# Optimization experiments

Hardware: AMD Instinct MI355X
Metric: run time of the kernel (lower is better)

The kernel has to match this reference:

```python
import jax, jax.numpy as jnp
import numpy as np

CONV_LAYERS = 1
BI_GRU_LAYERS = 2
BN_EPS = 1e-3


def _bn(x, gamma, beta, mean, var):
    return gamma * (x - mean) * jax.lax.rsqrt(var + BN_EPS) + beta


def _gru_pass(x, Wx, Wh, b_in, b_rec, reverse=False):
    # Keras GRU: reset_after=True, recurrent_activation=sigmoid, activation=relu,
    # gate order [z, r, h]. x: [B,T,D] -> [B,T,U]
    B, T, _ = x.shape
    U = Wh.shape[0]
    if reverse:
        x = x[:, ::-1]
    xg = jnp.einsum('btd,dg->btg', x, Wx) + b_in  # [B,T,3U] input-side gates, precomputed
    xg = jnp.swapaxes(xg, 0, 1)                    # time-major [T,B,3U]

    def step(h, g):
        rg = h @ Wh + b_rec                        # recurrent-side gates [B,3U]
        xz, xr, xh = jnp.split(g, 3, axis=-1)
        rz, rr, rh = jnp.split(rg, 3, axis=-1)
        z = jax.nn.sigmoid(xz + rz)
        r = jax.nn.sigmoid(xr + rr)
        hh = jax.nn.relu(xh + r * rh)              # reset_after: r gates the recurrent term
        h = z * h + (1.0 - z) * hh
        return h, h

    h0 = jnp.zeros((B, U), x.dtype)
    _, hs = jax.lax.scan(step, h0, xg)             # [T,B,U]
    hs = jnp.swapaxes(hs, 0, 1)
    if reverse:
        hs = hs[:, ::-1]
    return hs


def setup_inputs() -> dict:
    key = jax.random.key(0)
    ks = jax.random.split(key, 16)
    B, T, F = 32, 1024, 80
    C, U, V, K = 512, 512, 1024, 11
    s = 0.02
    inp = {
        'x': jax.random.normal(ks[0], (B, T, F), jnp.float32),
        'conv_w': jax.random.normal(ks[1], (K, F, C), jnp.float32) * s,
        'conv_b': jnp.zeros((C,), jnp.float32),
        'gru_fwd_wx': jax.random.normal(ks[2], (C, 3 * U), jnp.float32) * s,
        'gru_fwd_wh': jax.random.normal(ks[3], (U, 3 * U), jnp.float32) * s,
        'gru_fwd_bi': jnp.zeros((3 * U,), jnp.float32),
        'gru_fwd_br': jnp.zeros((3 * U,), jnp.float32),
        'gru_bwd_wx': jax.random.normal(ks[4], (C, 3 * U), jnp.float32) * s,
        'gru_bwd_wh': jax.random.normal(ks[5], (U, 3 * U), jnp.float32) * s,
        'gru_bwd_bi': jnp.zeros((3 * U,), jnp.float32),
        'gru_bwd_br': jnp.zeros((3 * U,), jnp.float32),
        'gamma': jnp.ones((C,), jnp.float32) + 0.1 * jax.random.normal(ks[6], (C,), jnp.float32),
        'beta': 0.1 * jax.random.normal(ks[7], (C,), jnp.float32),
        'mov_mean': jnp.zeros((C,), jnp.float32),
        'mov_var': jnp.ones((C,), jnp.float32),
        'dense_w': jax.random.normal(ks[8], (U, V), jnp.float32) * s,
        'dense_b': jnp.zeros((V,), jnp.float32),
    }
    return inp


def reference(x, conv_w, conv_b, gru_fwd_wx, gru_fwd_wh, gru_fwd_bi, gru_fwd_br,
              gru_bwd_wx, gru_bwd_wh, gru_bwd_bi, gru_bwd_br,
              gamma, beta, mov_mean, mov_var, dense_w, dense_b):
    for _ in range(CONV_LAYERS):
        x = jax.lax.conv_general_dilated(
            x, conv_w, window_strides=(2,), padding='SAME',
            dimension_numbers=('NWC', 'WIO', 'NWC'))
        x = jax.nn.relu(x + conv_b)
    x = _bn(x, gamma, beta, mov_mean, mov_var)  # same BN layer reused in source
    for _ in range(BI_GRU_LAYERS):              # same BiGRU layer (shared weights) reused
        x = (_gru_pass(x, gru_fwd_wx, gru_fwd_wh, gru_fwd_bi, gru_fwd_br, reverse=False)
             + _gru_pass(x, gru_bwd_wx, gru_bwd_wh, gru_bwd_bi, gru_bwd_br, reverse=True))
    x = _bn(x, gamma, beta, mov_mean, mov_var)
    logits = jnp.einsum('btu,uv->btv', x, dense_w) + dense_b
    return jax.nn.softmax(logits, axis=-1)
```

## Files before the change

### kernel.cpp

```cpp
#include <hip/hip_runtime.h>
#include <hip/hip_fp16.h>

#define BB 32
#define CC 512
#define UU 512
#define GG 1536
#define VV 1024
#define TT 512
#define MM (BB*TT)
#define TIN 1024
#define FIN 80
#define EPS 1e-3f
#define SENT 0xFFFFFFFFu

typedef _Float16 h8 __attribute__((ext_vector_type(8)));
typedef float f4 __attribute__((ext_vector_type(4)));

__global__ __launch_bounds__(256) void conv_bn_k(
    const float* __restrict__ x, const float* __restrict__ w, const float* __restrict__ cb,
    const float* __restrict__ gam, const float* __restrict__ bet,
    const float* __restrict__ mu_, const float* __restrict__ var_,
    __half* __restrict__ out)
{
  __shared__ float xs[41*80];
  int tg = blockIdx.x, b = blockIdx.y, ch = blockIdx.z;
  int t0 = tg*16;
  int in0 = t0*2 - 4;
  for (int i = threadIdx.x; i < 41*80; i += 256) {
    int r = i / 80, f = i - r*80;
    int ri = in0 + r;
    xs[i] = (ri >= 0 && ri < TIN) ? x[((size_t)b*TIN + ri)*FIN + f] : 0.f;
  }
  __syncthreads();
  int c = ch*256 + threadIdx.x;
  float acc[16];
  float bv = cb[c];
#pragma unroll
  for (int i = 0; i < 16; i++) acc[i] = bv;
  for (int k = 0; k < 11; k++) {
    for (int f = 0; f < 80; f++) {
      float wv = w[((size_t)k*80 + f)*CC + c];
#pragma unroll
      for (int i = 0; i < 16; i++) acc[i] += xs[(2*i + k)*80 + f] * wv;
    }
  }
  float ga = gam[c], be = bet[c], mu = mu_[c], iv = rsqrtf(var_[c] + EPS);
#pragma unroll
  for (int i = 0; i < 16; i++) {
    float v = fmaxf(acc[i], 0.f);
    out[((size_t)b*TT + t0 + i)*CC + c] = __float2half(ga*(v - mu)*iv + be);
  }
}

__global__ __launch_bounds__(256) void prep_wx_k(
    const float* __restrict__ wxf, const float* __restrict__ wxb,
    __half* __restrict__ of, __half* __restrict__ ob)
{
  __shared__ float tile[64][65];
  int kt = blockIdx.x*64, nt = blockIdx.y*64;
  const float* src = blockIdx.z ? wxb : wxf;
  __half* dst = blockIdx.z ? ob : of;
  for (int i = threadIdx.x; i < 4096; i += 256) {
    int r = i >> 6, c = i & 63;
    tile[r][c] = src[(size_t)(kt+r)*GG + nt + c];
  }
  __syncthreads();
  for (int i = threadIdx.x; i < 4096; i += 256) {
    int r = i >> 6, c = i & 63;
    __half h = __float2half(tile[c][r]);
    dst[(size_t)(nt+r)*1024 + kt + c] = h;
    dst[(size_t)(nt+r)*1024 + 512 + kt + c] = h;
  }
}

__global__ __launch_bounds__(256) void prep_dense_k(
    const float* __restrict__ dw, const float* __restrict__ gam, const float* __restrict__ var_,
    __half* __restrict__ dst)
{
  __shared__ float tile[64][65];
  __shared__ float s64[64];
  int kt = blockIdx.x*64, nt = blockIdx.y*64;
  if (threadIdx.x < 64) {
    int k = kt + threadIdx.x;
    s64[threadIdx.x] = gam[k] * rsqrtf(var_[k] + EPS);
  }
  for (int i = threadIdx.x; i < 4096; i += 256) {
    int r = i >> 6, c = i & 63;
    tile[r][c] = dw[(size_t)(kt+r)*VV + nt + c];
  }
  __syncthreads();
  for (int i = threadIdx.x; i < 4096; i += 256) {
    int r = i >> 6, c = i & 63;
    __half h = __float2half(tile[c][r] * s64[c]);
    dst[(size_t)(nt+r)*1024 + kt + c] = h;
    dst[(size_t)(nt+r)*1024 + 512 + kt + c] = h;
  }
}

__global__ __launch_bounds__(256) void prep_bias_k(
    const float* __restrict__ dw, const float* __restrict__ db,
    const float* __restrict__ gam, const float* __restrict__ bet,
    const float* __restrict__ mu_, const float* __restrict__ var_,
    float* __restrict__ bias2)
{
  int n = blockIdx.x*256 + threadIdx.x;
  float acc = db[n];
  for (int k = 0; k < CC; k++) {
    float o = bet[k] - gam[k]*mu_[k]*rsqrtf(var_[k] + EPS);
    acc += o * dw[(size_t)k*VV + n];
  }
  bias2[n] = acc;
}

template<int OUTH>
__global__ __launch_bounds__(256,2) void hgemm_k(
    const __half* __restrict__ A, const __half* __restrict__ BT,
    const float* __restrict__ bias, void* __restrict__ Cout,
    int M, int N, int K, int lda, int ldb)
{
  __shared__ _Float16 As[128*40];
  __shared__ _Float16 Bs[128*40];
  int m0 = blockIdx.y*128, n0 = blockIdx.x*128;
  int tid = threadIdx.x;
  int l = tid & 63, w = tid >> 6;
  int wr = w >> 1, wc = w & 1;
  int srow = tid >> 1, soff = (tid & 1)*16;
  const __half* ap = A  + (size_t)(m0 + srow)*lda + soff;
  const __half* bp = BT + (size_t)(n0 + srow)*ldb + soff;
  f4 acc[4][4];
#pragma unroll
  for (int i=0;i<4;i++)
#pragma unroll
    for (int j=0;j<4;j++) acc[i][j] = (f4){0.f,0.f,0.f,0.f};

  uint4 av  = *(const uint4*)(ap);
  uint4 av2 = *(const uint4*)(ap + 8);
  uint4 bv  = *(const uint4*)(bp);
  uint4 bv2 = *(const uint4*)(bp + 8);
  int lr = (l & 15), lk = (l >> 4)*8;
  for (int k0 = 0; k0 < K; k0 += 32) {
    __syncthreads();
    *(uint4*)&As[srow*40 + soff]     = av;
    *(uint4*)&As[srow*40 + soff + 8] = av2;
    *(uint4*)&Bs[srow*40 + soff]     = bv;
    *(uint4*)&Bs[srow*40 + soff + 8] = bv2;
    __syncthreads();
    if (k0 + 32 < K) {
      av  = *(const uint4*)(ap + k0 + 32);
      av2 = *(const uint4*)(ap + k0 + 40);
      bv  = *(const uint4*)(bp + k0 + 32);
      bv2 = *(const uint4*)(bp + k0 + 40);
    }
    h8 af[4], bf[4];
#pragma unroll
    for (int i = 0; i < 4; i++)
      af[i] = *(const h8*)&As[(wr*64 + i*16 + lr)*40 + lk];
#pragma unroll
    for (int j = 0; j < 4; j++)
      bf[j] = *(const h8*)&Bs[(wc*64 + j*16 + lr)*40 + lk];
#pragma unroll
    for (int i = 0; i < 4; i++)
#pragma unroll
      for (int j = 0; j < 4; j++)
        acc[i][j] = __builtin_amdgcn_mfma_f32_16x16x32_f16(af[i], bf[j], acc[i][j], 0, 0, 0);
  }
  int cb = n0 + wc*64 + lr;
  int rb = m0 + wr*64 + (l >> 4)*4;
#pragma unroll
  for (int j = 0; j < 4; j++) {
    float bs = bias[cb + j*16];
#pragma unroll
    for (int i = 0; i < 4; i++) {
#pragma unroll
      for (int q = 0; q < 4; q++) {
        float v = acc[i][j][q] + bs;
        int row = rb + i*16 + q, col = cb + j*16;
        if (OUTH) ((__half*)Cout)[(size_t)row*N + col] = __float2half(v);
        else      ((float*)Cout)[(size_t)row*N + col] = v;
      }
    }
  }
}

__global__ __launch_bounds__(256,1) void gru_layer_k(
    const __half* __restrict__ xgf, const __half* __restrict__ xgb,
    const float* __restrict__ whf, const float* __restrict__ whb,
    const float* __restrict__ brf, const float* __restrict__ brb,
    __half* __restrict__ H,
    unsigned* __restrict__ hbL)
{
  int wg  = blockIdx.x & 7;
  int bg  = (blockIdx.x >> 3) & 3;
  int dir = blockIdx.x >> 5;
  int grp = dir*4 + bg;
  const __half* xg = dir ? xgb : xgf;
  const float* wh  = dir ? whb : whf;
  const float* brc = dir ? brb : brf;
  unsigned* hbg = hbL + (size_t)grp*8192;
  int tid = threadIdx.x;
  int L = tid & 63, wv = tid >> 6;
  int u0 = wg*64, b0 = bg*8;

  __shared__ _Float16 hsl[2][8][544];

  int urow = L & 15, kb = L >> 4;
  int ubase = u0 + wv*16;
  h8 wb[3][16];
#pragma unroll
  for (int g3 = 0; g3 < 3; g3++)
#pragma unroll
    for (int ks = 0; ks < 16; ks++) {
      h8 v;
#pragma unroll
      for (int j = 0; j < 8; j++)
        v[j] = (_Float16)wh[(size_t)(ks*32 + kb*8 + j)*GG + g3*512 + ubase + urow];
      wb[g3][ks] = v;
    }

  int b = L & 15, b7 = L & 7;
  int myu = ubase + kb*4;
  float br3[3][4];
#pragma unroll
  for (int g3 = 0; g3 < 3; g3++)
#pragma unroll
    for (int q = 0; q < 4; q++)
      br3[g3][q] = brc[g3*512 + myu + q];
  float hreg[4] = {0.f, 0.f, 0.f, 0.f};
  bool bval = b < 8;
  int upair = (u0 >> 1) + wv*8 + kb*2;

  uint2 xz2, xr2, xh2;
  {
    int t0_ = dir ? 511 : 0;
    const unsigned* xp = (const unsigned*)xg + (size_t)((b0 + b7)*TT + t0_)*768;
    xz2 = *(const uint2*)(xp + upair);
    xr2 = *(const uint2*)(xp + 256 + upair);
    xh2 = *(const uint2*)(xp + 512 + upair);
  }

  (void)__hip_atomic_exchange(&hbg[0*2048 + wg*256 + tid], 0u,
                              __ATOMIC_RELAXED, __HIP_MEMORY_SCOPE_AGENT);

  int sr = tid >> 5, sc = tid & 31;
  int sb = sc >> 2, sg0 = sr*8 + (sc & 3)*2;
  int sws0 = ((sg0 ^ sb) << 3), sws1 = (((sg0 + 1) ^ sb) << 3);

#define STAGE(PH, NB) {                                                     \
    const unsigned* gp = &hbg[(PH)*2048 + sr*256 + sc*8];                   \
    uint4 d0, d1;                                                           \
    long guard = 0;                                                         \
    for (;;) {                                                              \
      asm volatile(                                                         \
        "global_load_dwordx4 %0, %2, off sc0 sc1\n\t"                       \
        "global_load_dwordx4 %1, %2, off offset:16 sc0 sc1\n\t"             \
        "s_waitcnt vmcnt(0)"                                                \
        : "=&v"(d0), "=&v"(d1) : "v"(gp) : "memory");                       \
      bool ok = (d0.x!=SENT)&(d0.y!=SENT)&(d0.z!=SENT)&(d0.w!=SENT)         \
              & (d1.x!=SENT)&(d1.y!=SENT)&(d1.z!=SENT)&(d1.w!=SENT);        \
      if (ok || ++guard > 3000000L) break;                                  \
    }                                                                       \
    *(uint4*)&hsl[NB][sb][sws0] = d0;                                       \
    *(uint4*)&hsl[NB][sb][sws1] = d1;                                       \
  }

  STAGE(0, 0);
  __syncthreads();

  for (int s = 0; s < 512; s++) {
    int buf = s & 1;
    (void)__hip_atomic_exchange(&hbg[((s+3)&3)*2048 + wg*256 + tid], SENT,
                                __ATOMIC_RELAXED, __HIP_MEMORY_SCOPE_AGENT);
    f4 a0 = (f4){0.f,0.f,0.f,0.f}, a1 = a0, a2 = a0;
#pragma unroll
    for (int ks = 0; ks < 16; ks++) {
      int g = ks*4 + kb;
      h8 hf = *(const h8*)&hsl[buf][b7][(g ^ b7) << 3];
      a0 = __builtin_amdgcn_mfma_f32_16x16x32_f16(wb[0][ks], hf, a0, 0, 0, 0);
      a1 = __builtin_amdgcn_mfma_f32_16x16x32_f16(wb[1][ks], hf, a1, 0, 0, 0);
      a2 = __builtin_amdgcn_mfma_f32_16x16x32_f16(wb[2][ks], hf, a2, 0, 0, 0);
    }
    int t = dir ? (511 - s) : s;
    __half2 xzl = *(__half2*)&xz2.x, xzh = *(__half2*)&xz2.y;
    __half2 xrl = *(__half2*)&xr2.x, xrh = *(__half2*)&xr2.y;
    __half2 xhl = *(__half2*)&xh2.x, xhh = *(__half2*)&xh2.y;
    float2 fz0 = __half22float2(xzl), fz1 = __half22float2(xzh);
    float2 fr0 = __half22float2(xrl), fr1 = __half22float2(xrh);
    float2 fh0 = __half22float2(xhl), fh1 = __half22float2(xhh);
    float xzf[4] = {fz0.x, fz0.y, fz1.x, fz1.y};
    float xrf[4] = {fr0.x, fr0.y, fr1.x, fr1.y};
    float xhf[4] = {fh0.x, fh0.y, fh1.x, fh1.y};
#pragma unroll
    for (int q = 0; q < 4; q++) {
      float az = (q==0? a0[0] : q==1? a0[1] : q==2? a0[2] : a0[3]);
      float ar = (q==0? a1[0] : q==1? a1[1] : q==2? a1[2] : a1[3]);
      float ah = (q==0? a2[0] : q==1? a2[1] : q==2? a2[2] : a2[3]);
      float z = 1.f/(1.f + __expf(-(xzf[q] + br3[0][q] + az)));
      float r = 1.f/(1.f + __expf(-(xrf[q] + br3[1][q] + ar)));
      float hh = fmaxf(xhf[q] + r*(br3[2][q] + ah), 0.f);
      hreg[q] = z*hreg[q] + (1.f - z)*hh;
    }
    int pn = (s + 1) & 3;
    if (bval) {
      __half2 p01 = __floats2half2_rn(hreg[0], hreg[1]);
      __half2 p23 = __floats2half2_rn(hreg[2], hreg[3]);
      unsigned pk0 = *(unsigned*)&p01, pk1 = *(unsigned*)&p23;
      unsigned long long pkl = ((unsigned long long)pk1 << 32) | pk0;
      (void)__hip_atomic_exchange(
          (unsigned long long*)&hbg[pn*2048 + wg*256 + b*32 + wv*8 + kb*2],
          pkl, __ATOMIC_RELAXED, __HIP_MEMORY_SCOPE_AGENT);
      uint2 pv; pv.x = pk0; pv.y = pk1;
      *(uint2*)((unsigned*)H + (size_t)((b0 + b)*TT + t)*512 + dir*256 + upair) = pv;
    }
    {
      int tn = (dir ? (510 - s) : (s + 1)) & 511;
      const unsigned* xp = (const unsigned*)xg + (size_t)((b0 + b7)*TT + tn)*768;
      xz2 = *(const uint2*)(xp + upair);
      xr2 = *(const uint2*)(xp + 256 + upair);
      xh2 = *(const uint2*)(xp + 512 + upair);
    }
    if (s < 511) STAGE(pn, buf ^ 1);
    __syncthreads();
  }
#undef STAGE
}

__global__ __launch_bounds__(256) void softmax_k(float* __restrict__ p) {
  size_t row = blockIdx.x;
  float* pr = p + row*VV;
  int tid = threadIdx.x;
  float4 v = ((float4*)pr)[tid];
  float m = fmaxf(fmaxf(v.x, v.y), fmaxf(v.z, v.w));
#pragma unroll
  for (int o = 32; o >= 1; o >>= 1) m = fmaxf(m, __shfl_xor(m, o));
  __shared__ float red[4];
  __shared__ float red2[4];
  int w = tid >> 6;
  if ((tid & 63) == 0) red[w] = m;
  __syncthreads();
  m = fmaxf(fmaxf(red[0], red[1]), fmaxf(red[2], red[3]));
  v.x = __expf(v.x - m); v.y = __expf(v.y - m);
  v.z = __expf(v.z - m); v.w = __expf(v.w - m);
  float s = v.x + v.y + v.z + v.w;
#pragma unroll
  for (int o = 32; o >= 1; o >>= 1) s += __shfl_xor(s, o);
  if ((tid & 63) == 0) red2[w] = s;
  __syncthreads();
  s = red2[0] + red2[1] + red2[2] + red2[3];
  float inv = 1.f / s;
  v.x *= inv; v.y *= inv; v.z *= inv; v.w *= inv;
  ((float4*)pr)[tid] = v;
}

extern "C" void kernel_launch(void* const* d_in, const int* in_sizes, int n_in,
                              void* d_out, int out_size, void* d_ws, size_t ws_size,
                              hipStream_t stream) {
  const float* x      = (const float*)d_in[0];
  const float* conv_w = (const float*)d_in[1];
  const float* conv_b = (const float*)d_in[2];
  const float* wx_f   = (const float*)d_in[3];
  const float* wh_f   = (const float*)d_in[4];
  const float* bi_f   = (const float*)d_in[5];
  const float* br_f   = (const float*)d_in[6];
  const float* wx_b   = (const float*)d_in[7];
  const float* wh_b   = (const float*)d_in[8];
  const float* bi_b   = (const float*)d_in[9];
  const float* br_b   = (const float*)d_in[10];
  const float* gam    = (const float*)d_in[11];
  const float* bet    = (const float*)d_in[12];
  const float* mu_    = (const float*)d_in[13];
  const float* var_   = (const float*)d_in[14];
  const float* dw     = (const float*)d_in[15];
  const float* db     = (const float*)d_in[16];

  char* ws = (char*)d_ws;
  __half* xgf   = (__half*)(ws + 0);
  __half* xgb   = (__half*)(ws + 50331648LL);
  __half* WxfT2 = (__half*)(ws + 100663296LL);
  __half* WxbT2 = (__half*)(ws + 103809024LL);
  __half* DwT2  = (__half*)(ws + 106954752LL);
  float*  bias2 = (float*)(ws + 109051904LL);
  __half* c0    = (__half*)(ws + 109056000LL);
  __half* H     = (__half*)(ws + 109056000LL);
  unsigned* hb1 = (unsigned*)(ws + 142610432LL);
  unsigned* hb2 = (unsigned*)(ws + 142872576LL);
  if (ws_size < 143134720ULL) return;
  float* logits = (float*)d_out;

  hipMemsetAsync(hb1, 0xFF, 524288, stream);

  prep_wx_k<<<dim3(8,24,2), 256, 0, stream>>>(wx_f, wx_b, WxfT2, WxbT2);
  prep_dense_k<<<dim3(8,16), 256, 0, stream>>>(dw, gam, var_, DwT2);
  prep_bias_k<<<4, 256, 0, stream>>>(dw, db, gam, bet, mu_, var_, bias2);

  conv_bn_k<<<dim3(32,32,2), 256, 0, stream>>>(x, conv_w, conv_b, gam, bet, mu_, var_, c0);

  hgemm_k<1><<<dim3(12,128), 256, 0, stream>>>(c0, WxfT2, bi_f, xgf, MM, GG, 512, 512, 1024);
  hgemm_k<1><<<dim3(12,128), 256, 0, stream>>>(c0, WxbT2, bi_b, xgb, MM, GG, 512, 512, 1024);
  gru_layer_k<<<64, 256, 0, stream>>>(xgf, xgb, wh_f, wh_b, br_f, br_b, H, hb1);
  hgemm_k<1><<<dim3(12,128), 256, 0, stream>>>(H, WxfT2, bi_f, xgf, MM, GG, 1024, 1024, 1024);
  hgemm_k<1><<<dim3(12,128), 256, 0, stream>>>(H, WxbT2, bi_b, xgb, MM, GG, 1024, 1024, 1024);
  gru_layer_k<<<64, 256, 0, stream>>>(xgf, xgb, wh_f, wh_b, br_f, br_b, H, hb2);
  hgemm_k<0><<<dim3(8,128), 256, 0, stream>>>(H, DwT2, bias2, logits, MM, VV, 1024, 1024, 1024);
  softmax_k<<<MM, 256, 0, stream>>>(logits);
}
```

Measured before the change: 2.840 ms.

## Double-buffer GEMM shared tiles and move GRU sentinel reset off critical path

The hgemm kernel now uses two shared-memory tile buffers, writing the next K-slice after the MFMA loop so each iteration needs one barrier instead of two. In the GRU recurrence, the sentinel reset of the slot three steps ahead moves from the start of each step to after staging, using 64-bit atomics from half the threads. The spin-wait adds s_sleep after a few failed polls to cut memory traffic from polling. Doubled LDS use may lower GEMM occupancy, and the sleep may add wake-up latency on the serial recurrence path.

Result: no change. 2.832 ms (-0.3%).

```diff
diff --git a/kernel.cpp b/kernel.cpp
--- a/kernel.cpp
+++ b/kernel.cpp
@@ -118,8 +118,8 @@
     const float* __restrict__ bias, void* __restrict__ Cout,
     int M, int N, int K, int lda, int ldb)
 {
-  __shared__ _Float16 As[128*40];
-  __shared__ _Float16 Bs[128*40];
+  __shared__ _Float16 As[2][128*40];
+  __shared__ _Float16 Bs[2][128*40];
   int m0 = blockIdx.y*128, n0 = blockIdx.x*128;
   int tid = threadIdx.x;
   int l = tid & 63, w = tid >> 6;
@@ -137,32 +137,41 @@
   uint4 av2 = *(const uint4*)(ap + 8);
   uint4 bv  = *(const uint4*)(bp);
   uint4 bv2 = *(const uint4*)(bp + 8);
+  *(uint4*)&As[0][srow*40 + soff]     = av;
+  *(uint4*)&As[0][srow*40 + soff + 8] = av2;
+  *(uint4*)&Bs[0][srow*40 + soff]     = bv;
+  *(uint4*)&Bs[0][srow*40 + soff + 8] = bv2;
+  __syncthreads();
+
   int lr = (l & 15), lk = (l >> 4)*8;
-  for (int k0 = 0; k0 < K; k0 += 32) {
-    __syncthreads();
-    *(uint4*)&As[srow*40 + soff]     = av;
-    *(uint4*)&As[srow*40 + soff + 8] = av2;
-    *(uint4*)&Bs[srow*40 + soff]     = bv;
-    *(uint4*)&Bs[srow*40 + soff + 8] = bv2;
-    __syncthreads();
-    if (k0 + 32 < K) {
-      av  = *(const uint4*)(ap + k0 + 32);
-      av2 = *(const uint4*)(ap + k0 + 40);
-      bv  = *(const uint4*)(bp + k0 + 32);
-      bv2 = *(const uint4*)(bp + k0 + 40);
+  int nk = K >> 5;
+  for (int kt = 0; kt < nk; kt++) {
+    int cb_ = kt & 1;
+    if (kt + 1 < nk) {
+      av  = *(const uint4*)(ap + kt*32 + 32);
+      av2 = *(const uint4*)(ap + kt*32 + 40);
+      bv  = *(const uint4*)(bp + kt*32 + 32);
+      bv2 = *(const uint4*)(bp + kt*32 + 40);
     }
     h8 af[4], bf[4];
 #pragma unroll
     for (int i = 0; i < 4; i++)
-      af[i] = *(const h8*)&As[(wr*64 + i*16 + lr)*40 + lk];
+      af[i] = *(const h8*)&As[cb_][(wr*64 + i*16 + lr)*40 + lk];
 #pragma unroll
     for (int j = 0; j < 4; j++)
-      bf[j] = *(const h8*)&Bs[(wc*64 + j*16 + lr)*40 + lk];
+      bf[j] = *(const h8*)&Bs[cb_][(wc*64 + j*16 + lr)*40 + lk];
 #pragma unroll
     for (int i = 0; i < 4; i++)
 #pragma unroll
       for (int j = 0; j < 4; j++)
         acc[i][j] = __builtin_amdgcn_mfma_f32_16x16x32_f16(af[i], bf[j], acc[i][j], 0, 0, 0);
+    if (kt + 1 < nk) {
+      *(uint4*)&As[cb_^1][srow*40 + soff]     = av;
+      *(uint4*)&As[cb_^1][srow*40 + soff + 8] = av2;
+      *(uint4*)&Bs[cb_^1][srow*40 + soff]     = bv;
+      *(uint4*)&Bs[cb_^1][srow*40 + soff + 8] = bv2;
+    }
+    __syncthreads();
   }
   int cb = n0 + wc*64 + lr;
   int rb = m0 + wr*64 + (l >> 4)*4;
@@ -257,7 +266,8 @@
         : "=&v"(d0), "=&v"(d1) : "v"(gp) : "memory");                       \
       bool ok = (d0.x!=SENT)&(d0.y!=SENT)&(d0.z!=SENT)&(d0.w!=SENT)         \
               & (d1.x!=SENT)&(d1.y!=SENT)&(d1.z!=SENT)&(d1.w!=SENT);        \
-      if (ok || ++guard > 3000000L) break;                                  \
+      if (ok || ++guard > 2000000L) break;                                  \
+      if (guard > 2) __builtin_amdgcn_s_sleep(1);                           \
     }                                                                       \
     *(uint4*)&hsl[NB][sb][sws0] = d0;                                       \
     *(uint4*)&hsl[NB][sb][sws1] = d1;                                       \
@@ -268,8 +278,6 @@
 
   for (int s = 0; s < 512; s++) {
     int buf = s & 1;
-    (void)__hip_atomic_exchange(&hbg[((s+3)&3)*2048 + wg*256 + tid], SENT,
-                                __ATOMIC_RELAXED, __HIP_MEMORY_SCOPE_AGENT);
     f4 a0 = (f4){0.f,0.f,0.f,0.f}, a1 = a0, a2 = a0;
 #pragma unroll
     for (int ks = 0; ks < 16; ks++) {
@@ -319,6 +327,10 @@
       xh2 = *(const uint2*)(xp + 512 + upair);
     }
     if (s < 511) STAGE(pn, buf ^ 1);
+    if (tid < 128)
+      (void)__hip_atomic_exchange(
+          (unsigned long long*)&hbg[((s+3)&3)*2048 + wg*256] + tid,
+          0xFFFFFFFFFFFFFFFFull, __ATOMIC_RELAXED, __HIP_MEMORY_SCOPE_AGENT);
     __syncthreads();
   }
 #undef STAGE
@@ -386,7 +398,7 @@
   if (ws_size < 143134720ULL) return;
   float* logits = (float*)d_out;
 
-  hipMemsetAsync(hb1, 0xFF, 524288, stream);
+  (void)hipMemsetAsync(hb1, 0xFF, 524288, stream);
 
   prep_wx_k<<<dim3(8,24,2), 256, 0, stream>>>(wx_f, wx_b, WxfT2, WxbT2);
   prep_dense_k<<<dim3(8,16), 256, 0, stream>>>(dw, gam, var_, DwT2);
```
